# Kernel tuning notes

Measured on AMD Instinct MI355X. Metric: run time of the kernel, lower is better.

Reference implementation:

```python
import jax, jax.numpy as jnp
import numpy as np

B, N, C, NC = 16, 49, 512, 12  # batch, spatial tokens, channels, num AU classes
EPS = 1e-5


def bn(h, axes):
    # torch BatchNorm (training mode, gamma=1, beta=0): biased batch stats
    m = h.mean(axes, keepdims=True)
    v = h.var(axes, keepdims=True)
    return (h - m) * jax.lax.rsqrt(v + EPS)


def cross_attn(y, x, qw, qb, kw, kb, vw, vb):
    # CrossAttn: q from y, k/v from x; attention over the token (N) axis
    q = y @ qw.T + qb            # (..., N, C//2)
    k = x @ kw.T + kb
    v = x @ vw.T + vb            # (..., N, C)
    scale = (C // 2) ** -0.5
    attn = jax.nn.softmax(jnp.einsum('...ij,...kj->...ik', q, k) * scale, axis=-1)
    return attn @ v


def _gnn_block(x, edge, A, Bm, E, U, V):
    # One ME-GraphAU GCN message-passing block.
    # x: (B, NC, C) node feats; edge: (B, NC*NC, C), edge (i,j) stored at i*NC+j
    b = x.shape[0]
    Vix = x @ A.T   # gathered at end node j of each edge
    Vjx = x @ Bm.T  # gathered at start node i of each edge
    msg = (Vjx[:, :, None, :] + Vix[:, None, :, :]).reshape(b, NC * NC, C) + edge @ E.T
    edge = edge + jax.nn.relu(bn(msg, (0, 2)))              # bne: per-edge-slot stats
    e = jax.nn.sigmoid(edge).reshape(b, NC, NC, C)
    e = jax.nn.softmax(e, axis=2)                            # softmax over target j
    Ujx = x @ V.T                                            # start-node features
    agg = (e * Ujx[:, :, None, :]).sum(axis=1) / NC          # sum over source i -> node j
    xn = x @ U.T + agg
    x = jax.nn.relu(x + bn(xn, (0, 2)))                      # bnv: per-class stats
    return x, edge


def _forward(x, cls_w, cls_b, attn_qw, attn_qb, attn_kw, attn_kb, attn_vw, attn_vb,
             ep_w, ep_b, gnn_w, mlp_w1, mlp_b1, mlp_w2, mlp_b2, mlp_w3, mlp_b3,
             final_w, final_b):
    b = x.shape[0]
    # per-class LinearBlocks, batched: (B, NC, N, C)
    h = jnp.einsum('bnc,koc->bkno', x, cls_w) + cls_b[None, :, None, :]
    f_u = jax.nn.relu(bn(h, (0, 2)))           # each class has its own BN over (B, N)
    f_v = f_u.mean(-2)                          # (B, NC, C)

    # GEM edge extractor
    g = jnp.broadcast_to(x[:, None], (b, NC, N, C))
    feat = cross_attn(f_u, g, attn_qw[0], attn_qb[0], attn_kw[0], attn_kb[0], attn_vw[0], attn_vb[0])
    # feat_end[i*NC+j] = feat[i]; feat_start[i*NC+j] = feat[j]
    feat_end = jnp.broadcast_to(feat[:, :, None], (b, NC, NC, N, C)).reshape(b, NC * NC, N, C)
    feat_start = jnp.broadcast_to(feat[:, None, :], (b, NC, NC, N, C)).reshape(b, NC * NC, N, C)
    feat2 = cross_attn(feat_start, feat_end, attn_qw[1], attn_qb[1], attn_kw[1], attn_kb[1], attn_vw[1], attn_vb[1])
    edge = bn(feat2 @ ep_w.T + ep_b, (0, 2, 3))  # BatchNorm2d(NC*NC): stats over (B, N, C)
    f_e = edge.mean(-2)                           # (B, NC*NC, C)

    # two GCN message-passing blocks
    U1, V1, A1, B1, E1, U2, V2, A2, B2, E2 = gnn_w
    f_v, f_e = _gnn_block(f_v, f_e, A1, B1, E1, U1, V1)
    f_v, f_e = _gnn_block(f_v, f_e, A2, B2, E2, U2, V2)

    # vectorized pairwise class-link head (feed_type='vertex+edge'), pairs i<j in loop order
    iu, ju = np.triu_indices(NC, 1)
    edges = jnp.concatenate([f_e[:, iu * NC + ju], f_e[:, ju * NC + iu]], axis=-1)  # (B, 66, 2C)
    nodes = jnp.concatenate([f_v[:, iu], f_v[:, ju]], axis=-1)                       # (B, 66, 2C)

    def mlp(z, i):
        z = jax.nn.relu(z @ mlp_w1[i].T + mlp_b1[i])
        z = jax.nn.relu(z @ mlp_w2[i].T + mlp_b2[i])
        return z @ mlp_w3[i].T + mlp_b3[i]

    ed = mlp(edges, 0)
    nd = mlp(nodes, 1)
    return jnp.concatenate([ed, nd], axis=-1) @ final_w.T + final_b  # (B, 66, 4)


def setup_inputs() -> dict:
    key = jax.random.key(0)
    ks = jax.random.split(key, 12)

    def w(k, shape, fan_in):
        return jax.random.normal(k, shape, jnp.float32) * (2.0 / fan_in) ** 0.5

    return dict(
        x=jax.random.normal(ks[0], (B, N, C), jnp.float32),
        cls_w=w(ks[1], (NC, C, C), C),          # per-class Linear (out, in)
        cls_b=jnp.zeros((NC, C), jnp.float32),
        attn_qw=w(ks[2], (2, C // 2, C), C),    # [0]=FAM, [1]=ARM
        attn_qb=jnp.zeros((2, C // 2), jnp.float32),
        attn_kw=w(ks[3], (2, C // 2, C), C),
        attn_kb=jnp.zeros((2, C // 2), jnp.float32),
        attn_vw=w(ks[4], (2, C, C), C),
        attn_vb=jnp.zeros((2, C), jnp.float32),
        ep_w=w(ks[5], (C, C), C),               # GEM edge_proj
        ep_b=jnp.zeros((C,), jnp.float32),
        gnn_w=w(ks[6], (10, C, C), C),          # U1,V1,A1,B1,E1,U2,V2,A2,B2,E2 (no bias)
        mlp_w1=w(ks[7], (2, C, 2 * C), 2 * C),  # [0]=edge_fc_*, [1]=node_fc_*
        mlp_b1=jnp.zeros((2, C), jnp.float32),
        mlp_w2=w(ks[8], (2, C // 2, C), C),
        mlp_b2=jnp.zeros((2, C // 2), jnp.float32),
        mlp_w3=w(ks[9], (2, 4, C // 2), C // 2),
        mlp_b3=jnp.zeros((2, 4), jnp.float32),
        final_w=w(ks[10], (4, 8), 8),
        final_b=jnp.zeros((4,), jnp.float32),
    )


def reference(x, cls_w, cls_b, attn_qw, attn_qb, attn_kw, attn_kb, attn_vw, attn_vb,
              ep_w, ep_b, gnn_w, mlp_w1, mlp_b1, mlp_w2, mlp_b2, mlp_w3, mlp_b3,
              final_w, final_b):
    return _forward(x, cls_w, cls_b, attn_qw, attn_qb, attn_kw, attn_kb, attn_vw, attn_vb,
                    ep_w, ep_b, gnn_w, mlp_w1, mlp_b1, mlp_w2, mlp_b2, mlp_w3, mlp_b3,
                    final_w, final_b)
```

## Files before the change

### kernel.cpp

```cpp
#include <hip/hip_runtime.h>

#define BN_EPS 1e-5f

typedef float f32x4 __attribute__((ext_vector_type(4)));
typedef short s16x8 __attribute__((ext_vector_type(8)));

__device__ __forceinline__ short f2bf(float f) {
    unsigned u = __builtin_bit_cast(unsigned, f);
    u = (u + 0x7fffu + ((u >> 16) & 1u)) >> 16;
    return (short)u;
}

template<int OMODE>
__global__ __launch_bounds__(256) void mfma_linear_kernel(
    const float* __restrict__ X, int Xstride,
    const float* __restrict__ W, int Wstride,
    const float* __restrict__ bias, int bstride,
    void* __restrict__ Yv, int Ystride,
    int R, int Cin, int Cout, int relu)
{
    const int mat = blockIdx.z;
    X += (size_t)mat * Xstride;
    W += (size_t)mat * Wstride;
    const float* bp = bias ? bias + mat * bstride : nullptr;
    float* Yf = (float*)Yv + (size_t)mat * Ystride;
    short* Ys = (short*)Yv + (size_t)mat * Ystride;

    const int r0 = blockIdx.y * 64;
    const int o0 = blockIdx.x * 64;

    __shared__ short As[64 * 40];
    __shared__ short Bs[64 * 40];

    const int tid = threadIdx.x;
    const int lane = tid & 63;
    const int wave = tid >> 6;
    const int wr = wave >> 1, wc = wave & 1;
    const int l15 = lane & 15;
    const int lk = lane >> 4;

    const int trow = tid >> 2;
    const int tseg = (tid & 3) * 8;

    f32x4 acc[2][2] = {};

    const int arow = r0 + trow;
    const bool aok = arow < R;
    const float* xrow = X + (size_t)arow * Cin + tseg;
    const float* wrow = W + (size_t)(o0 + trow) * Cin + tseg;

    for (int k0 = 0; k0 < Cin; k0 += 32) {
        float4 a0 = {}, a1 = {};
        if (aok) {
            a0 = *reinterpret_cast<const float4*>(xrow + k0);
            a1 = *reinterpret_cast<const float4*>(xrow + k0 + 4);
        }
        float4 b0 = *reinterpret_cast<const float4*>(wrow + k0);
        float4 b1 = *reinterpret_cast<const float4*>(wrow + k0 + 4);
        s16x8 av, bv;
        av[0] = f2bf(a0.x); av[1] = f2bf(a0.y); av[2] = f2bf(a0.z); av[3] = f2bf(a0.w);
        av[4] = f2bf(a1.x); av[5] = f2bf(a1.y); av[6] = f2bf(a1.z); av[7] = f2bf(a1.w);
        bv[0] = f2bf(b0.x); bv[1] = f2bf(b0.y); bv[2] = f2bf(b0.z); bv[3] = f2bf(b0.w);
        bv[4] = f2bf(b1.x); bv[5] = f2bf(b1.y); bv[6] = f2bf(b1.z); bv[7] = f2bf(b1.w);
        *reinterpret_cast<s16x8*>(&As[trow * 40 + tseg]) = av;
        *reinterpret_cast<s16x8*>(&Bs[trow * 40 + tseg]) = bv;
        __syncthreads();

        s16x8 af[2], bf[2];
        #pragma unroll
        for (int mi = 0; mi < 2; mi++)
            af[mi] = *reinterpret_cast<const s16x8*>(&As[(wr * 32 + mi * 16 + l15) * 40 + lk * 8]);
        #pragma unroll
        for (int ni = 0; ni < 2; ni++)
            bf[ni] = *reinterpret_cast<const s16x8*>(&Bs[(wc * 32 + ni * 16 + l15) * 40 + lk * 8]);
        #pragma unroll
        for (int mi = 0; mi < 2; mi++)
            #pragma unroll
            for (int ni = 0; ni < 2; ni++)
                acc[mi][ni] = __builtin_amdgcn_mfma_f32_16x16x32_bf16(af[mi], bf[ni], acc[mi][ni], 0, 0, 0);
        __syncthreads();
    }

    #pragma unroll
    for (int mi = 0; mi < 2; mi++) {
        #pragma unroll
        for (int ni = 0; ni < 2; ni++) {
            int col = o0 + wc * 32 + ni * 16 + l15;
            int row0 = r0 + wr * 32 + mi * 16 + lk * 4;
            float bb = bp ? bp[col] : 0.f;
            #pragma unroll
            for (int r = 0; r < 4; r++) {
                int row = row0 + r;
                if (row < R) {
                    float v = acc[mi][ni][r] + bb;
                    if (relu) v = fmaxf(v, 0.f);
                    if (OMODE == 0) {
                        Yf[(size_t)row * Cout + col] = v;
                    } else if (OMODE == 1) {
                        Ys[(size_t)row * Cout + col] = f2bf(v);
                    } else {
                        int t = row / 49, n = row - t * 49;
                        Ys[((size_t)t * 512 + col) * 64 + n] = f2bf(v);
                    }
                }
            }
        }
    }
}

__global__ __launch_bounds__(256) void bn1_partial_kernel(
    const float* __restrict__ h, float* __restrict__ bsum, float* __restrict__ bsq)
{
    int k = blockIdx.x;
    int part = blockIdx.y;
    int tid = threadIdx.x;
    #pragma unroll
    for (int half = 0; half < 2; half++) {
        int o = tid + half * 256;
        const float* base = h + (size_t)k * 401408 + (size_t)part * 98 * 512 + o;
        float s = 0.f, sq = 0.f;
        #pragma unroll 7
        for (int bn = 0; bn < 98; bn++) {
            float v = base[bn * 512];
            s += v; sq += v * v;
        }
        atomicAdd(&bsum[k * 512 + o], s);
        atomicAdd(&bsq[k * 512 + o], sq);
    }
}

__global__ __launch_bounds__(256) void fu_fv_kernel(
    float* __restrict__ h, const float* __restrict__ bsum,
    const float* __restrict__ bsq, float* __restrict__ f_v)
{
    int b = blockIdx.x;
    int k = blockIdx.y;
    int tid = threadIdx.x;
    #pragma unroll
    for (int half = 0; half < 2; half++) {
        int o = tid + half * 256;
        float mu = bsum[k * 512 + o] * (1.f / 784.f);
        float var = bsq[k * 512 + o] * (1.f / 784.f) - mu * mu;
        float rs = rsqrtf(var + BN_EPS);
        float* base = h + (size_t)(k * 16 + b) * 49 * 512 + o;
        float acc = 0.f;
        #pragma unroll 7
        for (int n = 0; n < 49; n++) {
            float v = (base[n * 512] - mu) * rs;
            v = fmaxf(v, 0.f);
            base[n * 512] = v;
            acc += v;
        }
        f_v[(b * 12 + k) * 512 + o] = acc * (1.f / 49.f);
    }
}

__global__ __launch_bounds__(256) void attn1_kernel(
    const float* __restrict__ q1,
    const float* __restrict__ k1,
    const float* __restrict__ v1,
    float* __restrict__ feat)
{
    int b = blockIdx.x;
    int k = blockIdx.y;
    __shared__ float ks[49 * 260];
    __shared__ float Pt[49 * 56];
    int tid = threadIdx.x;
    const float* kb = k1 + b * 49 * 256;
    for (int e = tid; e < 49 * 256; e += 256) ks[(e >> 8) * 260 + (e & 255)] = kb[e];
    __syncthreads();
    const float* qb = q1 + (k * 16 + b) * 49 * 256;
    for (int e = tid; e < 49 * 49; e += 256) {
        int qi = e / 49, kj = e - qi * 49;
        const float4* q4 = reinterpret_cast<const float4*>(qb + qi * 256);
        const float4* k4 = reinterpret_cast<const float4*>(ks + kj * 260);
        float s = 0.f;
        #pragma unroll 8
        for (int d = 0; d < 64; d++) {
            float4 a = q4[d], c = k4[d];
            s += a.x * c.x + a.y * c.y + a.z * c.z + a.w * c.w;
        }
        Pt[kj * 56 + qi] = s * 0.0625f;
    }
    __syncthreads();
    if (tid < 196) {
        int qi = tid >> 2, sub = tid & 3;
        float ev[13];
        float m = -1e30f;
        #pragma unroll 13
        for (int t = 0; t < 13; t++) {
            int j = sub + t * 4;
            ev[t] = (j < 49) ? Pt[j * 56 + qi] : -1e30f;
            m = fmaxf(m, ev[t]);
        }
        m = fmaxf(m, __shfl_xor(m, 1));
        m = fmaxf(m, __shfl_xor(m, 2));
        float s = 0.f;
        #pragma unroll 13
        for (int t = 0; t < 13; t++) { ev[t] = __expf(ev[t] - m); s += ev[t]; }
        s += __shfl_xor(s, 1);
        s += __shfl_xor(s, 2);
        float inv = 1.f / s;
        #pragma unroll 13
        for (int t = 0; t < 13; t++) {
            int j = sub + t * 4;
            if (j < 49) Pt[j * 56 + qi] = ev[t] * inv;
        }
    }
    __syncthreads();
    const float* vb = v1 + b * 49 * 512;
    float* fb = feat + (k * 16 + b) * 49 * 512;
    for (int qc = 0; qc < 49; qc += 8) {
        int nq = 49 - qc; if (nq > 8) nq = 8;
        float a0[8] = {}, a1[8] = {};
        for (int kj = 0; kj < 49; kj++) {
            float v0 = vb[kj * 512 + tid];
            float v1v = vb[kj * 512 + 256 + tid];
            const float4* pr = reinterpret_cast<const float4*>(&Pt[kj * 56 + qc]);
            float4 p0 = pr[0], p1 = pr[1];
            a0[0] += p0.x * v0; a1[0] += p0.x * v1v;
            a0[1] += p0.y * v0; a1[1] += p0.y * v1v;
            a0[2] += p0.z * v0; a1[2] += p0.z * v1v;
            a0[3] += p0.w * v0; a1[3] += p0.w * v1v;
            a0[4] += p1.x * v0; a1[4] += p1.x * v1v;
            a0[5] += p1.y * v0; a1[5] += p1.y * v1v;
            a0[6] += p1.z * v0; a1[6] += p1.z * v1v;
            a0[7] += p1.w * v0; a1[7] += p1.w * v1v;
        }
        #pragma unroll 8
        for (int u = 0; u < 8; u++) {
            if (u < nq) {
                fb[(qc + u) * 512 + tid] = a0[u];
                fb[(qc + u) * 512 + 256 + tid] = a1[u];
            }
        }
    }
}

__global__ __launch_bounds__(256) void attn2_mfma_kernel(
    const short* __restrict__ q2,
    const short* __restrict__ k2,
    const short* __restrict__ w2vT,
    const float* __restrict__ ep_b,
    float* __restrict__ fe_raw,
    float* __restrict__ stats)
{
    const int b = blockIdx.x, i = blockIdx.y, j = blockIdx.z;
    __shared__ float S[64 * 68];
    __shared__ short P[64 * 88];
    __shared__ float red[256];
    const int tid = threadIdx.x;
    const int lane = tid & 63, w = tid >> 6;
    const int l15 = lane & 15, lk = lane >> 4;

    const short* qb = q2 + (size_t)((j * 16 + b) * 49) * 256;
    const short* kb = k2 + (size_t)((i * 16 + b) * 49) * 256;

    {
        int qrow = w * 16 + l15; if (qrow > 48) qrow = 48;
        f32x4 sacc[4] = {};
        #pragma unroll
        for (int ks = 0; ks < 8; ks++) {
            s16x8 aq = *reinterpret_cast<const s16x8*>(qb + (size_t)qrow * 256 + ks * 32 + lk * 8);
            #pragma unroll
            for (int ni = 0; ni < 4; ni++) {
                int krow = ni * 16 + l15; if (krow > 48) krow = 48;
                s16x8 bk = *reinterpret_cast<const s16x8*>(kb + (size_t)krow * 256 + ks * 32 + lk * 8);
                sacc[ni] = __builtin_amdgcn_mfma_f32_16x16x32_bf16(aq, bk, sacc[ni], 0, 0, 0);
            }
        }
        #pragma unroll
        for (int ni = 0; ni < 4; ni++)
            #pragma unroll
            for (int r = 0; r < 4; r++)
                S[(w * 16 + lk * 4 + r) * 68 + ni * 16 + l15] = sacc[ni][r] * 0.0625f;
    }
    __syncthreads();

    if (tid < 196) {
        int qi = tid >> 2, sub = tid & 3;
        float ev[13];
        float m = -1e30f;
        #pragma unroll 13
        for (int t = 0; t < 13; t++) {
            int kk = sub + t * 4;
            ev[t] = (kk < 49) ? S[qi * 68 + kk] : -1e30f;
            m = fmaxf(m, ev[t]);
        }
        m = fmaxf(m, __shfl_xor(m, 1));
        m = fmaxf(m, __shfl_xor(m, 2));
        float s = 0.f;
        #pragma unroll 13
        for (int t = 0; t < 13; t++) { ev[t] = __expf(ev[t] - m); s += ev[t]; }
        s += __shfl_xor(s, 1);
        s += __shfl_xor(s, 2);
        float inv = 1.f / s;
        #pragma unroll 13
        for (int t = 0; t < 13; t++) {
            int kk = sub + t * 4;
            if (kk < 49) P[qi * 88 + kk] = f2bf(ev[t] * inv);
        }
        for (int kk = 49 + sub; kk < 64; kk += 4) P[qi * 88 + kk] = 0;
    } else {
        int t2 = tid - 196;
        for (int idx = t2; idx < 15 * 64; idx += 60) {
            int rr = idx / 64, cc = idx - rr * 64;
            P[(49 + rr) * 88 + cc] = 0;
        }
    }
    __syncthreads();

    const short* vt = w2vT + (size_t)((i * 16 + b) * 512) * 64;
    const int slot = i * 12 + j;
    float tot = 0.f, csq = 0.f;
    #pragma unroll
    for (int half = 0; half < 2; half++) {
        const int cb = half * 256 + w * 64;
        f32x4 pac[4][4] = {};
        #pragma unroll
        for (int ks = 0; ks < 2; ks++) {
            s16x8 bv[4];
            #pragma unroll
            for (int ni = 0; ni < 4; ni++) {
                int ch = cb + ni * 16 + l15;
                bv[ni] = *reinterpret_cast<const s16x8*>(vt + (size_t)ch * 64 + ks * 32 + lk * 8);
            }
            #pragma unroll
            for (int mi = 0; mi < 4; mi++) {
                s16x8 ap = *reinterpret_cast<const s16x8*>(&P[(mi * 16 + l15) * 88 + ks * 32 + lk * 8]);
                #pragma unroll
                for (int ni = 0; ni < 4; ni++)
                    pac[mi][ni] = __builtin_amdgcn_mfma_f32_16x16x32_bf16(ap, bv[ni], pac[mi][ni], 0, 0, 0);
            }
        }
        #pragma unroll
        for (int ni = 0; ni < 4; ni++) {
            int col = cb + ni * 16 + l15;
            float bias = ep_b[col];
            float cs = 0.f;
            #pragma unroll
            for (int mi = 0; mi < 4; mi++) {
                #pragma unroll
                for (int r = 0; r < 4; r++) {
                    int row = mi * 16 + lk * 4 + r;
                    if (row < 49) {
                        float sv = pac[mi][ni][r] + bias;
                        cs += sv; csq += sv * sv;
                    }
                }
            }
            tot += cs;
            cs += __shfl_xor(cs, 16);
            cs += __shfl_xor(cs, 32);
            if (lk == 0)
                fe_raw[((size_t)b * 144 + slot) * 512 + col] = cs * (1.f / 49.f);
        }
    }
    red[tid] = tot; __syncthreads();
    for (int t = 128; t > 0; t >>= 1) { if (tid < t) red[tid] += red[tid + t]; __syncthreads(); }
    if (tid == 0) atomicAdd(&stats[slot * 2], red[0]);
    __syncthreads();
    red[tid] = csq; __syncthreads();
    for (int t = 128; t > 0; t >>= 1) { if (tid < t) red[tid] += red[tid + t]; __syncthreads(); }
    if (tid == 0) atomicAdd(&stats[slot * 2 + 1], red[0]);
}

__global__ __launch_bounds__(256) void edge_fin_kernel(
    const float* __restrict__ stats, float* __restrict__ fe)
{
    int s = blockIdx.x;
    const float inv = 1.f / 401408.f;
    float mu = stats[s * 2] * inv;
    float var = stats[s * 2 + 1] * inv - mu * mu;
    float rs = rsqrtf(var + BN_EPS);
    int tid = threadIdx.x;
    for (int b = 0; b < 16; b++) {
        float* p = fe + (b * 144 + s) * 512;
        #pragma unroll
        for (int half = 0; half < 2; half++) {
            int c = tid + half * 256;
            p[c] = (p[c] - mu) * rs;
        }
    }
}

__global__ __launch_bounds__(256) void gnn_edge_kernel(
    const float* __restrict__ nodeproj,
    const float* __restrict__ eE,
    float* __restrict__ fe)
{
    int s = blockIdx.x;
    int i = s / 12, j = s - i * 12;
    int tid = threadIdx.x;
    const float* Vix = nodeproj + 2 * 98304;
    const float* Vjx = nodeproj + 3 * 98304;
    __shared__ float red[256];
    float msg[32];
    float sum = 0.f, sq = 0.f;
    int idx = 0;
    for (int b = 0; b < 16; b++) {
        #pragma unroll
        for (int half = 0; half < 2; half++) {
            int c = tid + half * 256;
            float v = Vjx[(b * 12 + i) * 512 + c] + Vix[(b * 12 + j) * 512 + c]
                    + eE[(b * 144 + s) * 512 + c];
            msg[idx++] = v;
            sum += v; sq += v * v;
        }
    }
    red[tid] = sum; __syncthreads();
    for (int t = 128; t > 0; t >>= 1) { if (tid < t) red[tid] += red[tid + t]; __syncthreads(); }
    float tsum = red[0]; __syncthreads();
    red[tid] = sq; __syncthreads();
    for (int t = 128; t > 0; t >>= 1) { if (tid < t) red[tid] += red[tid + t]; __syncthreads(); }
    float tsq = red[0];
    float mu = tsum * (1.f / 8192.f);
    float var = tsq * (1.f / 8192.f) - mu * mu;
    float rs = rsqrtf(var + BN_EPS);
    idx = 0;
    for (int b = 0; b < 16; b++) {
        #pragma unroll
        for (int half = 0; half < 2; half++) {
            int c = tid + half * 256;
            float v = fmaxf((msg[idx++] - mu) * rs, 0.f);
            fe[(b * 144 + s) * 512 + c] += v;
        }
    }
}

__global__ __launch_bounds__(256) void gnn_agg_kernel(
    const float* __restrict__ fe,
    const float* __restrict__ nodeproj,
    float* __restrict__ xn_agg)
{
    int b = blockIdx.x;
    int i = blockIdx.y;
    int tid = threadIdx.x;
    const float* Ujx = nodeproj + 98304;
    #pragma unroll
    for (int half = 0; half < 2; half++) {
        int c = tid + half * 256;
        float sg[12];
        float m = -1e30f;
        #pragma unroll
        for (int j = 0; j < 12; j++) {
            float e = fe[(b * 144 + i * 12 + j) * 512 + c];
            float sv = 1.f / (1.f + __expf(-e));
            sg[j] = sv;
            m = fmaxf(m, sv);
        }
        float ssum = 0.f;
        #pragma unroll
        for (int j = 0; j < 12; j++) { float evv = __expf(sg[j] - m); sg[j] = evv; ssum += evv; }
        float wgt = Ujx[(b * 12 + i) * 512 + c] / ssum;
        #pragma unroll
        for (int j = 0; j < 12; j++)
            atomicAdd(&xn_agg[(b * 12 + j) * 512 + c], sg[j] * wgt);
    }
}

__global__ __launch_bounds__(256) void gnn_node_kernel(
    const float* __restrict__ xn_agg, const float* __restrict__ nodeproj,
    float* __restrict__ fv)
{
    int k = blockIdx.x;
    int tid = threadIdx.x;
    const float* Ux = nodeproj;
    __shared__ float red[256];
    float vals[32];
    float sum = 0.f, sq = 0.f;
    int idx = 0;
    for (int b = 0; b < 16; b++) {
        #pragma unroll
        for (int half = 0; half < 2; half++) {
            int c = tid + half * 256;
            int o = (b * 12 + k) * 512 + c;
            float v = Ux[o] + xn_agg[o] * (1.f / 12.f);
            vals[idx++] = v;
            sum += v; sq += v * v;
        }
    }
    red[tid] = sum; __syncthreads();
    for (int t = 128; t > 0; t >>= 1) { if (tid < t) red[tid] += red[tid + t]; __syncthreads(); }
    float tsum = red[0]; __syncthreads();
    red[tid] = sq; __syncthreads();
    for (int t = 128; t > 0; t >>= 1) { if (tid < t) red[tid] += red[tid + t]; __syncthreads(); }
    float tsq = red[0];
    float mu = tsum * (1.f / 8192.f);
    float var = tsq * (1.f / 8192.f) - mu * mu;
    float rs = rsqrtf(var + BN_EPS);
    idx = 0;
    for (int b = 0; b < 16; b++) {
        #pragma unroll
        for (int half = 0; half < 2; half++) {
            int c = tid + half * 256;
            int o = (b * 12 + k) * 512 + c;
            float v = (vals[idx++] - mu) * rs;
            fv[o] = fmaxf(fv[o] + v, 0.f);
        }
    }
}

__global__ __launch_bounds__(256) void pair_gather_kernel(
    const float* __restrict__ fe, const float* __restrict__ fv, float* __restrict__ pairX)
{
    int p = blockIdx.x;
    int b = blockIdx.y;
    int tid = threadIdx.x;
    int i = 0, rem = p;
    while (rem >= 11 - i) { rem -= 11 - i; i++; }
    int j = i + 1 + rem;
    float* e_out = pairX + (b * 66 + p) * 1024;
    float* n_out = pairX + 1056 * 1024 + (b * 66 + p) * 1024;
    const float* fe_ij = fe + (b * 144 + i * 12 + j) * 512;
    const float* fe_ji = fe + (b * 144 + j * 12 + i) * 512;
    const float* fv_i = fv + (b * 12 + i) * 512;
    const float* fv_j = fv + (b * 12 + j) * 512;
    #pragma unroll
    for (int half = 0; half < 2; half++) {
        int c = tid + half * 256;
        e_out[c] = fe_ij[c];
        e_out[512 + c] = fe_ji[c];
        n_out[c] = fv_i[c];
        n_out[512 + c] = fv_j[c];
    }
}

__global__ __launch_bounds__(256) void mlp3_kernel(
    const float* __restrict__ X,
    const float* __restrict__ w3,
    const float* __restrict__ b3,
    float* __restrict__ Y)
{
    int idx = blockIdx.x * 256 + threadIdx.x;
    if (idx >= 8448) return;
    int o = idx & 3;
    int r = (idx >> 2) % 1056;
    int m = idx / (4 * 1056);
    const float* x = X + (m * 1056 + r) * 256;
    const float* w = w3 + (m * 4 + o) * 256;
    float s = b3[m * 4 + o];
    #pragma unroll 8
    for (int c = 0; c < 256; c++) s += x[c] * w[c];
    Y[idx] = s;
}

__global__ __launch_bounds__(256) void final_kernel(
    const float* __restrict__ mid3,
    const float* __restrict__ fw,
    const float* __restrict__ fb,
    float* __restrict__ out)
{
    int idx = blockIdx.x * 256 + threadIdx.x;
    if (idx >= 4224) return;
    int o = idx & 3;
    int r = idx >> 2;
    const float* ed = mid3 + r * 4;
    const float* nd = mid3 + 1056 * 4 + r * 4;
    float s = fb[o];
    #pragma unroll
    for (int q = 0; q < 4; q++) s += ed[q] * fw[o * 8 + q];
    #pragma unroll
    for (int q = 0; q < 4; q++) s += nd[q] * fw[o * 8 + 4 + q];
    out[idx] = s;
}

extern "C" void kernel_launch(void* const* d_in, const int* in_sizes, int n_in,
                              void* d_out, int out_size, void* d_ws, size_t ws_size,
                              hipStream_t stream)
{
    const float* x      = (const float*)d_in[0];
    const float* cls_w  = (const float*)d_in[1];
    const float* cls_b  = (const float*)d_in[2];
    const float* qw     = (const float*)d_in[3];
    const float* qb     = (const float*)d_in[4];
    const float* kw     = (const float*)d_in[5];
    const float* kb     = (const float*)d_in[6];
    const float* vw     = (const float*)d_in[7];
    const float* vb     = (const float*)d_in[8];
    const float* ep_w   = (const float*)d_in[9];
    const float* ep_b   = (const float*)d_in[10];
    const float* gnn_w  = (const float*)d_in[11];
    const float* mlp_w1 = (const float*)d_in[12];
    const float* mlp_b1 = (const float*)d_in[13];
    const float* mlp_w2 = (const float*)d_in[14];
    const float* mlp_b2 = (const float*)d_in[15];
    const float* mlp_w3 = (const float*)d_in[16];
    const float* mlp_b3 = (const float*)d_in[17];
    const float* fin_w  = (const float*)d_in[18];
    const float* fin_b  = (const float*)d_in[19];
    float* out = (float*)d_out;
    float* ws = (float*)d_ws;

    float* A     = ws;
    float* q1b   = A + 4816896;
    float* k1b   = q1b + 2408448;
    float* v1b   = k1b + 200704;
    float* Bb    = v1b + 401408;
    float* Cb    = Bb + 4816896;
    float* fv    = Cb + 4816896;
    float* bn1m  = fv + 98304;
    float* bn1r  = bn1m + 6144;
    float* fe    = bn1r + 6144;
    float* stats = fe + 1179648;

    short* q2bf = (short*)A;
    short* k2bf = (short*)(A + 1204224);
    float* v2b  = Cb;
    short* w2vT = (short*)Bb;

    float* nodeproj = Cb;
    float* eE       = Cb + 393216;
    float* xn       = Cb + 1572864;
    float* pairX = Cb;
    float* mid1  = Cb + 2162688;
    float* mid2  = Cb + 3244032;
    float* mid3  = Cb + 3784704;

    mfma_linear_kernel<0><<<dim3(8, 13, 12), 256, 0, stream>>>(x, 0, cls_w, 262144, cls_b, 512,
                                                               A, 401408, 784, 512, 512, 0);
    hipMemsetAsync(bn1m, 0, 2 * 6144 * sizeof(float), stream);
    bn1_partial_kernel<<<dim3(12, 8), 256, 0, stream>>>(A, bn1m, bn1r);
    fu_fv_kernel<<<dim3(16, 12), 256, 0, stream>>>(A, bn1m, bn1r, fv);
    mfma_linear_kernel<0><<<dim3(4, 147, 1), 256, 0, stream>>>(A, 0, qw, 0, qb, 0,
                                                               q1b, 0, 9408, 512, 256, 0);
    mfma_linear_kernel<0><<<dim3(4, 13, 1), 256, 0, stream>>>(x, 0, kw, 0, kb, 0,
                                                              k1b, 0, 784, 512, 256, 0);
    mfma_linear_kernel<0><<<dim3(8, 13, 1), 256, 0, stream>>>(x, 0, vw, 0, vb, 0,
                                                              v1b, 0, 784, 512, 512, 0);
    attn1_kernel<<<dim3(16, 12), 256, 0, stream>>>(q1b, k1b, v1b, Bb);
    mfma_linear_kernel<1><<<dim3(4, 147, 1), 256, 0, stream>>>(Bb, 0, qw + 131072, 0, qb + 256, 0,
                                                               q2bf, 0, 9408, 512, 256, 0);
    mfma_linear_kernel<1><<<dim3(4, 147, 1), 256, 0, stream>>>(Bb, 0, kw + 131072, 0, kb + 256, 0,
                                                               k2bf, 0, 9408, 512, 256, 0);
    mfma_linear_kernel<0><<<dim3(8, 147, 1), 256, 0, stream>>>(Bb, 0, vw + 262144, 0, vb + 512, 0,
                                                               v2b, 0, 9408, 512, 512, 0);
    hipMemsetAsync(w2vT, 0, (size_t)12 * 16 * 512 * 64 * sizeof(short), stream);
    mfma_linear_kernel<2><<<dim3(8, 147, 1), 256, 0, stream>>>(v2b, 0, ep_w, 0, nullptr, 0,
                                                               w2vT, 0, 9408, 512, 512, 0);
    hipMemsetAsync(stats, 0, 288 * sizeof(float), stream);
    attn2_mfma_kernel<<<dim3(16, 12, 12), 256, 0, stream>>>(q2bf, k2bf, w2vT, ep_b, fe, stats);
    edge_fin_kernel<<<144, 256, 0, stream>>>(stats, fe);

    for (int blk = 0; blk < 2; blk++) {
        const float* gw = gnn_w + blk * 5 * 262144;
        mfma_linear_kernel<0><<<dim3(8, 3, 4), 256, 0, stream>>>(fv, 0, gw, 262144, nullptr, 0,
                                                                 nodeproj, 98304, 192, 512, 512, 0);
        mfma_linear_kernel<0><<<dim3(8, 36, 1), 256, 0, stream>>>(fe, 0, gw + 4 * 262144, 0, nullptr, 0,
                                                                  eE, 0, 2304, 512, 512, 0);
        gnn_edge_kernel<<<144, 256, 0, stream>>>(nodeproj, eE, fe);
        hipMemsetAsync(xn, 0, 98304 * sizeof(float), stream);
        gnn_agg_kernel<<<dim3(16, 12), 256, 0, stream>>>(fe, nodeproj, xn);
        gnn_node_kernel<<<12, 256, 0, stream>>>(xn, nodeproj, fv);
    }

    pair_gather_kernel<<<dim3(66, 16), 256, 0, stream>>>(fe, fv, pairX);
    mfma_linear_kernel<0><<<dim3(8, 17, 2), 256, 0, stream>>>(pairX, 1081344, mlp_w1, 524288, mlp_b1, 512,
                                                              mid1, 540672, 1056, 1024, 512, 1);
    mfma_linear_kernel<0><<<dim3(4, 17, 2), 256, 0, stream>>>(mid1, 540672, mlp_w2, 131072, mlp_b2, 256,
                                                              mid2, 270336, 1056, 512, 256, 1);
    mlp3_kernel<<<33, 256, 0, stream>>>(mid2, mlp_w3, mlp_b3, mid3);
    final_kernel<<<17, 256, 0, stream>>>(mid3, fin_w, fin_b, out);
}
```

Measured before the change: 508.6 us.

## Stage per-(b,i) V tile in swizzled LDS and loop over j inside block

Each attn2 block now handles one (b,i) pair and loops over all 12 j values instead of using one block per (b,i,j). The 64KB w2vT slice is loaded once into LDS with an XOR swizzle and reused across the j iterations, and the zero padding of P is done once. The block-wide stats reduction through shared memory is replaced by wave-level shuffles plus per-wave atomics. The grid shrinks from 2304 blocks to 192, and the larger LDS footprint limits occupancy, so the kernel may lose latency hiding and parallelism.

```diff
diff --git a/kernel.cpp b/kernel.cpp
--- a/kernel.cpp
+++ b/kernel.cpp
@@ -245,124 +245,132 @@
     float* __restrict__ fe_raw,
     float* __restrict__ stats)
 {
-    const int b = blockIdx.x, i = blockIdx.y, j = blockIdx.z;
+    const int b = blockIdx.x, i = blockIdx.y;
+    __shared__ short Vs[512 * 64];
     __shared__ float S[64 * 68];
     __shared__ short P[64 * 88];
-    __shared__ float red[256];
     const int tid = threadIdx.x;
     const int lane = tid & 63, w = tid >> 6;
     const int l15 = lane & 15, lk = lane >> 4;
 
-    const short* qb = q2 + (size_t)((j * 16 + b) * 49) * 256;
+    {
+        const float4* src = reinterpret_cast<const float4*>(w2vT + (size_t)((i * 16 + b) * 512) * 64);
+        float4* dst = reinterpret_cast<float4*>(Vs);
+        #pragma unroll
+        for (int it = 0; it < 16; it++) {
+            int c = tid + it * 256;
+            int ch = c >> 3, c8 = c & 7;
+            dst[(ch << 3) | (c8 ^ (ch & 7))] = src[c];
+        }
+        for (int idx = tid; idx < 64 * 88; idx += 256) P[idx] = 0;
+    }
     const short* kb = k2 + (size_t)((i * 16 + b) * 49) * 256;
-
-    {
-        int qrow = w * 16 + l15; if (qrow > 48) qrow = 48;
-        f32x4 sacc[4] = {};
-        #pragma unroll
-        for (int ks = 0; ks < 8; ks++) {
-            s16x8 aq = *reinterpret_cast<const s16x8*>(qb + (size_t)qrow * 256 + ks * 32 + lk * 8);
+    __syncthreads();
+
+    for (int j = 0; j < 12; j++) {
+        const short* qb = q2 + (size_t)((j * 16 + b) * 49) * 256;
+        {
+            int qrow = w * 16 + l15; if (qrow > 48) qrow = 48;
+            f32x4 sacc[4] = {};
+            #pragma unroll
+            for (int ks = 0; ks < 8; ks++) {
+                s16x8 aq = *reinterpret_cast<const s16x8*>(qb + (size_t)qrow * 256 + ks * 32 + lk * 8);
+                #pragma unroll
+                for (int ni = 0; ni < 4; ni++) {
+                    int krow = ni * 16 + l15; if (krow > 48) krow = 48;
+                    s16x8 bk = *reinterpret_cast<const s16x8*>(kb + (size_t)krow * 256 + ks * 32 + lk * 8);
+                    sacc[ni] = __builtin_amdgcn_mfma_f32_16x16x32_bf16(aq, bk, sacc[ni], 0, 0, 0);
+                }
+            }
+            #pragma unroll
+            for (int ni = 0; ni < 4; ni++)
+                #pragma unroll
+                for (int r = 0; r < 4; r++)
+                    S[(w * 16 + lk * 4 + r) * 68 + ni * 16 + l15] = sacc[ni][r] * 0.0625f;
+        }
+        __syncthreads();
+
+        if (tid < 196) {
+            int qi = tid >> 2, sub = tid & 3;
+            float ev[13];
+            float m = -1e30f;
+            #pragma unroll 13
+            for (int t = 0; t < 13; t++) {
+                int kk = sub + t * 4;
+                ev[t] = (kk < 49) ? S[qi * 68 + kk] : -1e30f;
+                m = fmaxf(m, ev[t]);
+            }
+            m = fmaxf(m, __shfl_xor(m, 1));
+            m = fmaxf(m, __shfl_xor(m, 2));
+            float s = 0.f;
+            #pragma unroll 13
+            for (int t = 0; t < 13; t++) { ev[t] = __expf(ev[t] - m); s += ev[t]; }
+            s += __shfl_xor(s, 1);
+            s += __shfl_xor(s, 2);
+            float inv = 1.f / s;
+            #pragma unroll 13
+            for (int t = 0; t < 13; t++) {
+                int kk = sub + t * 4;
+                if (kk < 49) P[qi * 88 + kk] = f2bf(ev[t] * inv);
+            }
+        }
+        __syncthreads();
+
+        const int slot = i * 12 + j;
+        float tot = 0.f, csq = 0.f;
+        #pragma unroll
+        for (int half = 0; half < 2; half++) {
+            const int cb = half * 256 + w * 64;
+            f32x4 pac[4][4] = {};
+            #pragma unroll
+            for (int ks = 0; ks < 2; ks++) {
+                s16x8 bv[4];
+                #pragma unroll
+                for (int ni = 0; ni < 4; ni++) {
+                    int ch = cb + ni * 16 + l15;
+                    int boff = ((ch * 64 + ks * 32 + lk * 8) * 2) ^ ((ch & 7) << 4);
+                    bv[ni] = *reinterpret_cast<const s16x8*>(reinterpret_cast<const char*>(Vs) + boff);
+                }
+                #pragma unroll
+                for (int mi = 0; mi < 4; mi++) {
+                    s16x8 ap = *reinterpret_cast<const s16x8*>(&P[(mi * 16 + l15) * 88 + ks * 32 + lk * 8]);
+                    #pragma unroll
+                    for (int ni = 0; ni < 4; ni++)
+                        pac[mi][ni] = __builtin_amdgcn_mfma_f32_16x16x32_bf16(ap, bv[ni], pac[mi][ni], 0, 0, 0);
+                }
+            }
             #pragma unroll
             for (int ni = 0; ni < 4; ni++) {
-                int krow = ni * 16 + l15; if (krow > 48) krow = 48;
-                s16x8 bk = *reinterpret_cast<const s16x8*>(kb + (size_t)krow * 256 + ks * 32 + lk * 8);
-                sacc[ni] = __builtin_amdgcn_mfma_f32_16x16x32_bf16(aq, bk, sacc[ni], 0, 0, 0);
-            }
-        }
-        #pragma unroll
-        for (int ni = 0; ni < 4; ni++)
-            #pragma unroll
-            for (int r = 0; r < 4; r++)
-                S[(w * 16 + lk * 4 + r) * 68 + ni * 16 + l15] = sacc[ni][r] * 0.0625f;
-    }
-    __syncthreads();
-
-    if (tid < 196) {
-        int qi = tid >> 2, sub = tid & 3;
-        float ev[13];
-        float m = -1e30f;
-        #pragma unroll 13
-        for (int t = 0; t < 13; t++) {
-            int kk = sub + t * 4;
-            ev[t] = (kk < 49) ? S[qi * 68 + kk] : -1e30f;
-            m = fmaxf(m, ev[t]);
-        }
-        m = fmaxf(m, __shfl_xor(m, 1));
-        m = fmaxf(m, __shfl_xor(m, 2));
-        float s = 0.f;
-        #pragma unroll 13
-        for (int t = 0; t < 13; t++) { ev[t] = __expf(ev[t] - m); s += ev[t]; }
-        s += __shfl_xor(s, 1);
-        s += __shfl_xor(s, 2);
-        float inv = 1.f / s;
-        #pragma unroll 13
-        for (int t = 0; t < 13; t++) {
-            int kk = sub + t * 4;
-            if (kk < 49) P[qi * 88 + kk] = f2bf(ev[t] * inv);
-        }
-        for (int kk = 49 + sub; kk < 64; kk += 4) P[qi * 88 + kk] = 0;
-    } else {
-        int t2 = tid - 196;
-        for (int idx = t2; idx < 15 * 64; idx += 60) {
-            int rr = idx / 64, cc = idx - rr * 64;
-            P[(49 + rr) * 88 + cc] = 0;
-        }
-    }
-    __syncthreads();
-
-    const short* vt = w2vT + (size_t)((i * 16 + b) * 512) * 64;
-    const int slot = i * 12 + j;
-    float tot = 0.f, csq = 0.f;
-    #pragma unroll
-    for (int half = 0; half < 2; half++) {
-        const int cb = half * 256 + w * 64;
-        f32x4 pac[4][4] = {};
-        #pragma unroll
-        for (int ks = 0; ks < 2; ks++) {
-            s16x8 bv[4];
-            #pragma unroll
-            for (int ni = 0; ni < 4; ni++) {
-                int ch = cb + ni * 16 + l15;
-                bv[ni] = *reinterpret_cast<const s16x8*>(vt + (size_t)ch * 64 + ks * 32 + lk * 8);
-            }
-            #pragma unroll
-            for (int mi = 0; mi < 4; mi++) {
-                s16x8 ap = *reinterpret_cast<const s16x8*>(&P[(mi * 16 + l15) * 88 + ks * 32 + lk * 8]);
+                int col = cb + ni * 16 + l15;
+                float bias = ep_b[col];
+                float cs = 0.f;
                 #pragma unroll
-                for (int ni = 0; ni < 4; ni++)
-                    pac[mi][ni] = __builtin_amdgcn_mfma_f32_16x16x32_bf16(ap, bv[ni], pac[mi][ni], 0, 0, 0);
-            }
-        }
-        #pragma unroll
-        for (int ni = 0; ni < 4; ni++) {
-            int col = cb + ni * 16 + l15;
-            float bias = ep_b[col];
-            float cs = 0.f;
-            #pragma unroll
-            for (int mi = 0; mi < 4; mi++) {
-                #pragma unroll
-                for (int r = 0; r < 4; r++) {
-                    int row = mi * 16 + lk * 4 + r;
-                    if (row < 49) {
-                        float sv = pac[mi][ni][r] + bias;
-                        cs += sv; csq += sv * sv;
+                for (int mi = 0; mi < 4; mi++) {
+                    #pragma unroll
+                    for (int r = 0; r < 4; r++) {
+                        int row = mi * 16 + lk * 4 + r;
+                        if (row < 49) {
+                            float sv = pac[mi][ni][r] + bias;
+                            cs += sv; csq += sv * sv;
+                        }
                     }
                 }
+                tot += cs;
+                cs += __shfl_xor(cs, 16);
+                cs += __shfl_xor(cs, 32);
+                if (lk == 0)
+                    fe_raw[((size_t)b * 144 + slot) * 512 + col] = cs * (1.f / 49.f);
             }
-            tot += cs;
-            cs += __shfl_xor(cs, 16);
-            cs += __shfl_xor(cs, 32);
-            if (lk == 0)
-                fe_raw[((size_t)b * 144 + slot) * 512 + col] = cs * (1.f / 49.f);
-        }
-    }
-    red[tid] = tot; __syncthreads();
-    for (int t = 128; t > 0; t >>= 1) { if (tid < t) red[tid] += red[tid + t]; __syncthreads(); }
-    if (tid == 0) atomicAdd(&stats[slot * 2], red[0]);
-    __syncthreads();
-    red[tid] = csq; __syncthreads();
-    for (int t = 128; t > 0; t >>= 1) { if (tid < t) red[tid] += red[tid + t]; __syncthreads(); }
-    if (tid == 0) atomicAdd(&stats[slot * 2 + 1], red[0]);
+        }
+        tot += __shfl_xor(tot, 1);  tot += __shfl_xor(tot, 2);  tot += __shfl_xor(tot, 4);
+        tot += __shfl_xor(tot, 8);  tot += __shfl_xor(tot, 16); tot += __shfl_xor(tot, 32);
+        csq += __shfl_xor(csq, 1);  csq += __shfl_xor(csq, 2);  csq += __shfl_xor(csq, 4);
+        csq += __shfl_xor(csq, 8);  csq += __shfl_xor(csq, 16); csq += __shfl_xor(csq, 32);
+        if (lane == 0) {
+            atomicAdd(&stats[slot * 2], tot);
+            atomicAdd(&stats[slot * 2 + 1], csq);
+        }
+    }
 }
 
 __global__ __launch_bounds__(256) void edge_fin_kernel(
@@ -639,7 +647,7 @@
     mfma_linear_kernel<2><<<dim3(8, 147, 1), 256, 0, stream>>>(v2b, 0, ep_w, 0, nullptr, 0,
                                                                w2vT, 0, 9408, 512, 512, 0);
     hipMemsetAsync(stats, 0, 288 * sizeof(float), stream);
-    attn2_mfma_kernel<<<dim3(16, 12, 12), 256, 0, stream>>>(q2bf, k2bf, w2vT, ep_b, fe, stats);
+    attn2_mfma_kernel<<<dim3(16, 12), 256, 0, stream>>>(q2bf, k2bf, w2vT, ep_b, fe, stats);
     edge_fin_kernel<<<144, 256, 0, stream>>>(stats, fe);
 
     for (int blk = 0; blk < 2; blk++) {
```

New measurement: 496.7 us. 1.02x faster.
